# Kernel tuning notes

Measured on AMD Instinct MI355X. Metric: run time of the kernel, lower is better.

Reference implementation:

```python
import jax, jax.numpy as jnp
import numpy as np

N_NODES = 50000
N_RAND_EDGES = 800000  # plus N_NODES self-loop edges appended in setup
IN_FEATS, N_HIDDEN, N_CLASSES = 128, 64, 64


def setup_inputs() -> dict:
    key = jax.random.key(0)
    kf, ks, kd, k1, k2, k3 = jax.random.split(key, 6)
    features = jax.random.normal(kf, (N_NODES, IN_FEATS), dtype=jnp.float32)
    src = jax.random.randint(ks, (N_RAND_EDGES,), 0, N_NODES, dtype=jnp.int32)
    dst = jax.random.randint(kd, (N_RAND_EDGES,), 0, N_NODES, dtype=jnp.int32)
    # dgl.add_self_loop: append (i, i) for every node
    loop = jnp.arange(N_NODES, dtype=jnp.int32)
    src = jnp.concatenate([src, loop])
    dst = jnp.concatenate([dst, loop])

    def glorot(k, fan_in, fan_out):
        lim = jnp.sqrt(6.0 / (fan_in + fan_out)).astype(jnp.float32)
        return jax.random.uniform(k, (fan_in, fan_out), jnp.float32, -lim, lim)

    return {
        "features": features, "src": src, "dst": dst,
        "W1": glorot(k1, IN_FEATS, N_HIDDEN), "b1": jnp.zeros((N_HIDDEN,), jnp.float32),
        "W2": glorot(k2, N_HIDDEN, N_HIDDEN), "b2": jnp.zeros((N_HIDDEN,), jnp.float32),
        "W3": glorot(k3, N_HIDDEN, N_CLASSES), "b3": jnp.zeros((N_CLASSES,), jnp.float32),
    }


def _graph_conv(x, W, b, src, dst, norm_src_e, norm_dst_n, n_nodes):
    """DGL GraphConv, norm='both': D_dst^{-1/2} A D_src^{-1/2} X W + b, then relu."""
    if W.shape[0] > W.shape[1]:  # mult by W first when it shrinks the feature dim
        x = x @ W
        m = x[src] * norm_src_e[:, None]                      # [E, out]
        h = jax.ops.segment_sum(m, dst, num_segments=n_nodes)  # [N, out]
        h = h * norm_dst_n[:, None]
    else:
        m = x[src] * norm_src_e[:, None]                      # [E, in]
        h = jax.ops.segment_sum(m, dst, num_segments=n_nodes)  # [N, in]
        h = (h * norm_dst_n[:, None]) @ W
    return jax.nn.relu(h + b)


def reference(features, src, dst, W1, b1, W2, b2, W3, b3):
    n = features.shape[0]
    ones = jnp.ones(src.shape[0], dtype=features.dtype)
    out_deg = jax.ops.segment_sum(ones, src, num_segments=n)
    in_deg = jax.ops.segment_sum(ones, dst, num_segments=n)
    norm_out = jnp.where(out_deg > 0, jax.lax.rsqrt(jnp.maximum(out_deg, 1.0)), 0.0)
    norm_in = jnp.where(in_deg > 0, jax.lax.rsqrt(jnp.maximum(in_deg, 1.0)), 0.0)
    norm_src_e = norm_out[src]  # per-edge source normalization

    h1 = _graph_conv(features, W1, b1, src, dst, norm_src_e, norm_in, n)
    h2 = _graph_conv(h1, W2, b2, src, dst, norm_src_e, norm_in, n)
    h3 = _graph_conv(h2, W3, b3, src, dst, norm_src_e, norm_in, n)
    # JumpingKnowledge mode='max': elementwise max over stacked layer outputs
    return jnp.max(jnp.stack([h1, h2, h3], axis=0), axis=0)
```

## Files before the change

### kernel.cpp

```cpp
#include <hip/hip_runtime.h>

typedef _Float16 h16;
typedef __attribute__((ext_vector_type(4))) _Float16 half4;
typedef __attribute__((ext_vector_type(8))) _Float16 half8;
typedef __attribute__((ext_vector_type(8))) float float8;

#define RANGES 8
#define PPR    32
#define HTHREADS 1024
#define BINS   6400
#define HALF   (BINS / 2)
#define HWORDS (BINS)

__global__ __launch_bounds__(HTHREADS) void hist_kernel(const int* __restrict__ src,
                                                        const int* __restrict__ dst,
                                                        int* __restrict__ partial, int E) {
  __shared__ int h[HWORDS];
  const int r = blockIdx.x >> 5;
  const int c = blockIdx.x & 31;
  for (int i = threadIdx.x; i < HWORDS; i += HTHREADS) h[i] = 0;
  __syncthreads();
  const int lo = r * BINS;
  const int chunk = (E + PPR - 1) / PPR;
  const int e0 = c * chunk;
  const int e1 = min(E, e0 + chunk);
  for (int e = e0 + threadIdx.x; e < e1; e += HTHREADS) {
    int s = src[e] - lo;
    if ((unsigned)s < (unsigned)BINS) atomicAdd(&h[s >> 1], 1 << ((s & 1) * 16));
    int d = dst[e] - lo;
    if ((unsigned)d < (unsigned)BINS) atomicAdd(&h[HALF + (d >> 1)], 1 << ((d & 1) * 16));
  }
  __syncthreads();
  int* op = partial + (size_t)blockIdx.x * HWORDS;
  for (int i = threadIdx.x; i < HWORDS; i += HTHREADS) op[i] = h[i];
}

__global__ __launch_bounds__(256) void reduce_norm_scan1(
    int* __restrict__ partial, float* __restrict__ nout, float* __restrict__ nin,
    int* __restrict__ rowptr, int* __restrict__ bsums, int N) {
  __shared__ int s[256];
  const int j = blockIdx.x * 256 + threadIdx.x;
  const int r = j / HALF;
  const int w = j % HALF;
  int* base = partial + (size_t)(r * PPR) * HWORDS;
  int sumO = 0, runI = 0;
#pragma unroll 8
  for (int p = 0; p < PPR; ++p) {
    sumO += base[(size_t)p * HWORDS + w];
    int vI = base[(size_t)p * HWORDS + HALF + w];
    base[(size_t)p * HWORDS + HALF + w] = runI;
    runI += vI;
  }
  const int od0 = sumO & 0xFFFF, od1 = (sumO >> 16) & 0xFFFF;
  const int id0 = runI & 0xFFFF, id1 = (runI >> 16) & 0xFFFF;
  const int n0 = 2 * j, n1 = 2 * j + 1;
  if (n0 < N) {
    nout[n0] = od0 > 0 ? rsqrtf((float)od0) : 0.f;
    nin[n0]  = id0 > 0 ? rsqrtf((float)id0) : 0.f;
  }
  if (n1 < N) {
    nout[n1] = od1 > 0 ? rsqrtf((float)od1) : 0.f;
    nin[n1]  = id1 > 0 ? rsqrtf((float)id1) : 0.f;
  }
  const int local = id0 + id1;
  int v = local;
  s[threadIdx.x] = v;
  __syncthreads();
#pragma unroll
  for (int off = 1; off < 256; off <<= 1) {
    int tv = 0;
    if (threadIdx.x >= off) tv = s[threadIdx.x - off];
    __syncthreads();
    if (threadIdx.x >= off) s[threadIdx.x] += tv;
    __syncthreads();
  }
  const int excl = s[threadIdx.x] - v;
  if (n0 < N) rowptr[n0] = excl;
  if (n1 < N) rowptr[n1] = excl + id0;
  if (threadIdx.x == 255) bsums[blockIdx.x] = s[255];
}

__global__ __launch_bounds__(512) void add_off2(int* __restrict__ rowptr,
                                                const int* __restrict__ bsums,
                                                int N, int E, int nb) {
  __shared__ int s[128];
  const int tid = threadIdx.x;
  if (tid < 128) s[tid] = (tid < nb) ? bsums[tid] : 0;
  __syncthreads();
#pragma unroll
  for (int off = 1; off < 128; off <<= 1) {
    int v = 0;
    if (tid < 128 && tid >= off) v = s[tid - off];
    __syncthreads();
    if (tid < 128 && tid >= off) s[tid] += v;
    __syncthreads();
  }
  const int base = (blockIdx.x == 0) ? 0 : s[blockIdx.x - 1];
  const int i = blockIdx.x * 512 + tid;
  if (i < N) rowptr[i] += base;
  if (blockIdx.x == 0 && tid == 0) rowptr[N] = E;
}

__global__ __launch_bounds__(HTHREADS) void fill_kernel(
    const int* __restrict__ src, const int* __restrict__ dst,
    const int* __restrict__ rowptr, const int* __restrict__ partial,
    int* __restrict__ csr, int N, int E) {
  __shared__ int cur[BINS];
  const int r = blockIdx.x & 7;
  const int c = blockIdx.x >> 3;
  const int lo = r * BINS;
  const int* pf = partial + (size_t)(r * PPR + c) * HWORDS + HALF;
  for (int n = threadIdx.x; n < BINS; n += HTHREADS) {
    int g = lo + n;
    int rp = (g < N) ? rowptr[g] : 0;
    int pw = pf[n >> 1];
    cur[n] = rp + ((pw >> ((n & 1) * 16)) & 0xFFFF);
  }
  __syncthreads();
  const int chunk = (E + PPR - 1) / PPR;
  const int e0 = c * chunk;
  const int e1 = min(E, e0 + chunk);
  for (int e = e0 + threadIdx.x; e < e1; e += HTHREADS) {
    int d = dst[e] - lo;
    if ((unsigned)d < (unsigned)BINS) {
      int pos = atomicAdd(&cur[d], 1);
      csr[pos] = src[e];
    }
  }
}

__device__ __forceinline__ float8 gather_row(const int* __restrict__ rowptr,
                                             const int* __restrict__ csr,
                                             const half8* __restrict__ xv,
                                             int node, int lane) {
  const int b = rowptr[node], e = rowptr[node + 1];
  float8 a0 = 0.f, a1 = 0.f, a2 = 0.f, a3 = 0.f;
  int i = b;
  for (; i + 4 <= e; i += 4) {
    int s0 = csr[i + 0], s1 = csr[i + 1], s2 = csr[i + 2], s3 = csr[i + 3];
    half8 v0 = xv[(size_t)s0 * 8 + lane];
    half8 v1 = xv[(size_t)s1 * 8 + lane];
    half8 v2 = xv[(size_t)s2 * 8 + lane];
    half8 v3 = xv[(size_t)s3 * 8 + lane];
#pragma unroll
    for (int j = 0; j < 8; ++j) {
      a0[j] += (float)v0[j]; a1[j] += (float)v1[j];
      a2[j] += (float)v2[j]; a3[j] += (float)v3[j];
    }
  }
  for (; i < e; ++i) {
    int s = csr[i];
    half8 v = xv[(size_t)s * 8 + lane];
#pragma unroll
    for (int j = 0; j < 8; ++j) a0[j] += (float)v[j];
  }
#pragma unroll
  for (int j = 0; j < 8; ++j) a0[j] = (a0[j] + a1[j]) + (a2[j] + a3[j]);
  return a0;
}

__global__ __launch_bounds__(512) void agg1_kernel(
    const int* __restrict__ rowptr, const int* __restrict__ csr,
    const h16* __restrict__ x, const float* __restrict__ nin,
    const float* __restrict__ bias, const float* __restrict__ nout,
    half8* __restrict__ y, float* __restrict__ out, int N) {
  int t = blockIdx.x * 512 + threadIdx.x;
  int node = t >> 3;
  if (node >= N) return;
  int lane = t & 7;
  float8 acc = gather_row(rowptr, csr, reinterpret_cast<const half8*>(x), node, lane);
  const float s = nin[node];
  const float no = nout[node];
  float8 h;
  half8 hv;
#pragma unroll
  for (int j = 0; j < 8; ++j) {
    h[j] = fmaxf(acc[j] * s + bias[lane * 8 + j], 0.f);
    hv[j] = (h16)(h[j] * no);
  }
  float4 o0 = make_float4(h[0], h[1], h[2], h[3]);
  float4 o1 = make_float4(h[4], h[5], h[6], h[7]);
  size_t off = (size_t)node * 64 + lane * 8;
  *reinterpret_cast<float4*>(out + off)     = o0;
  *reinterpret_cast<float4*>(out + off + 4) = o1;
  y[(size_t)node * 8 + lane] = hv;
}

template <bool WRITEC>
__global__ __launch_bounds__(512) void fused_layer(
    const int* __restrict__ rowptr, const int* __restrict__ csr,
    const h16* __restrict__ x, const float* __restrict__ W,
    const float* __restrict__ nin, const float* __restrict__ bias,
    const float* __restrict__ nout,
    half4* __restrict__ C, float* __restrict__ out, int N) {
  __shared__ float sA[64][68];
  __shared__ float sB[64][64];
  const int t = threadIdx.x;
  const int row0 = blockIdx.x * 64;

  for (int i = t * 4; i < 64 * 64; i += 512 * 4)
    *reinterpret_cast<float4*>(&sB[0][0] + i) = *reinterpret_cast<const float4*>(W + i);

  {
    const int node = t >> 3, lane = t & 7;
    const int g = row0 + node;
    float8 acc = 0.f;
    float s = 0.f;
    if (g < N) {
      acc = gather_row(rowptr, csr, reinterpret_cast<const half8*>(x), g, lane);
      s = nin[g];
    }
    float4 w0 = make_float4(acc[0] * s, acc[1] * s, acc[2] * s, acc[3] * s);
    float4 w1 = make_float4(acc[4] * s, acc[5] * s, acc[6] * s, acc[7] * s);
    *reinterpret_cast<float4*>(&sA[node][lane * 8])     = w0;
    *reinterpret_cast<float4*>(&sA[node][lane * 8 + 4]) = w1;
  }
  __syncthreads();

  const int tx = t & 15;
  const int ry = t >> 4;
  const int r0 = 2 * ry, r1 = 2 * ry + 1;
  float4 acc0 = make_float4(0.f, 0.f, 0.f, 0.f);
  float4 acc1 = make_float4(0.f, 0.f, 0.f, 0.f);
#pragma unroll 8
  for (int k = 0; k < 64; ++k) {
    float a0 = sA[r0][k], a1 = sA[r1][k];
    float4 b = *reinterpret_cast<float4*>(&sB[k][tx * 4]);
    acc0.x += a0 * b.x; acc0.y += a0 * b.y; acc0.z += a0 * b.z; acc0.w += a0 * b.w;
    acc1.x += a1 * b.x; acc1.y += a1 * b.y; acc1.z += a1 * b.z; acc1.w += a1 * b.w;
  }

  const float4 bb = *reinterpret_cast<const float4*>(bias + tx * 4);
#pragma unroll
  for (int rr = 0; rr < 2; ++rr) {
    const int gr = row0 + (rr ? r1 : r0);
    if (gr >= N) continue;
    float4 v = rr ? acc1 : acc0;
    v.x = fmaxf(v.x + bb.x, 0.f);
    v.y = fmaxf(v.y + bb.y, 0.f);
    v.z = fmaxf(v.z + bb.z, 0.f);
    v.w = fmaxf(v.w + bb.w, 0.f);
    size_t off = (size_t)gr * 64 + tx * 4;
    float4 o = *reinterpret_cast<float4*>(out + off);
    o.x = fmaxf(o.x, v.x);
    o.y = fmaxf(o.y, v.y);
    o.z = fmaxf(o.z, v.z);
    o.w = fmaxf(o.w, v.w);
    *reinterpret_cast<float4*>(out + off) = o;
    if (WRITEC) {
      float no = nout[gr];
      half4 hv;
      hv.x = (h16)(v.x * no); hv.y = (h16)(v.y * no);
      hv.z = (h16)(v.z * no); hv.w = (h16)(v.w * no);
      C[(size_t)gr * 16 + tx] = hv;
    }
  }
}

__global__ __launch_bounds__(256) void gemm1_kernel(
    const float* __restrict__ A, const float* __restrict__ B,
    const float* __restrict__ nout, half4* __restrict__ C, int M) {
  __shared__ float sA[64][132];
  __shared__ float sB[128][64];
  const int t = threadIdx.x;
  const int row0 = blockIdx.x * 64;

  for (int i = t * 4; i < 64 * 128; i += 256 * 4) {
    int r = i / 128, c = i % 128;
    int gr = row0 + r;
    float4 v = make_float4(0.f, 0.f, 0.f, 0.f);
    if (gr < M) v = *reinterpret_cast<const float4*>(A + (size_t)gr * 128 + c);
    *reinterpret_cast<float4*>(&sA[r][c]) = v;
  }
  for (int i = t * 4; i < 128 * 64; i += 256 * 4)
    *reinterpret_cast<float4*>(&sB[0][0] + i) = *reinterpret_cast<const float4*>(B + i);
  __syncthreads();

  const int ty = t >> 4;
  const int tx = t & 15;
  float acc[4][4] = {};
#pragma unroll 8
  for (int k = 0; k < 128; ++k) {
    float a[4];
#pragma unroll
    for (int i = 0; i < 4; ++i) a[i] = sA[ty * 4 + i][k];
    float4 b = *reinterpret_cast<float4*>(&sB[k][tx * 4]);
#pragma unroll
    for (int i = 0; i < 4; ++i) {
      acc[i][0] += a[i] * b.x;
      acc[i][1] += a[i] * b.y;
      acc[i][2] += a[i] * b.z;
      acc[i][3] += a[i] * b.w;
    }
  }

#pragma unroll
  for (int i = 0; i < 4; ++i) {
    int gr = row0 + ty * 4 + i;
    if (gr >= M) continue;
    float no = nout[gr];
    half4 hv;
    hv.x = (h16)(acc[i][0] * no); hv.y = (h16)(acc[i][1] * no);
    hv.z = (h16)(acc[i][2] * no); hv.w = (h16)(acc[i][3] * no);
    C[(size_t)gr * 16 + tx] = hv;
  }
}

extern "C" void kernel_launch(void* const* d_in, const int* in_sizes, int n_in,
                              void* d_out, int out_size, void* d_ws, size_t ws_size,
                              hipStream_t stream) {
  const float* feat = (const float*)d_in[0];
  const int* src    = (const int*)d_in[1];
  const int* dst    = (const int*)d_in[2];
  const float* W1   = (const float*)d_in[3];
  const float* b1   = (const float*)d_in[4];
  const float* W2   = (const float*)d_in[5];
  const float* b2   = (const float*)d_in[6];
  const float* W3   = (const float*)d_in[7];
  const float* b3   = (const float*)d_in[8];
  float* out = (float*)d_out;

  const int N = in_sizes[0] / 128;
  const int E = in_sizes[1];

  char* p = (char*)d_ws;
  float* nout   = (float*)p;          p += (size_t)N * 4;
  float* nin    = (float*)p;          p += (size_t)N * 4;
  int*   rowptr = (int*)p;            p += ((size_t)N + 8) * 4;
  int*   bsums  = (int*)p;            p += 1024 * 4;
  int*   csr    = (int*)p;            p += (size_t)E * 4;
  p = (char*)(((uintptr_t)p + 15) & ~(uintptr_t)15);
  h16*   bufAh  = (h16*)p;            p += (size_t)N * 64 * 2;
  h16*   bufBh  = (h16*)p;            p += (size_t)N * 64 * 2;
  int*   partial = (int*)bufAh;

  const int nwords = RANGES * HALF;
  const int nb = nwords / 256;

  hist_kernel<<<RANGES * PPR, HTHREADS, 0, stream>>>(src, dst, partial, E);
  reduce_norm_scan1<<<nb, 256, 0, stream>>>(partial, nout, nin, rowptr, bsums, N);
  add_off2<<<nb, 512, 0, stream>>>(rowptr, bsums, N, E, nb);
  fill_kernel<<<RANGES * PPR, HTHREADS, 0, stream>>>(src, dst, rowptr, partial, csr, N, E);

  const int gemm_blocks  = (N + 63) / 64;
  const int agg1_blocks  = (int)(((size_t)N * 8 + 511) / 512);

  gemm1_kernel<<<gemm_blocks, 256, 0, stream>>>(feat, W1, nout, (half4*)bufAh, N);
  agg1_kernel<<<agg1_blocks, 512, 0, stream>>>(rowptr, csr, bufAh, nin, b1, nout,
                                               (half8*)bufBh, out, N);

  fused_layer<true><<<gemm_blocks, 512, 0, stream>>>(rowptr, csr, bufBh, W2, nin, b2, nout,
                                                     (half4*)bufAh, out, N);

  fused_layer<false><<<gemm_blocks, 512, 0, stream>>>(rowptr, csr, bufAh, W3, nin, b3, nullptr,
                                                      nullptr, out, N);
}
```

Before: 167.3 us.

## Merge all stages into one cooperative persistent kernel with grid syncs

Replaces the eight separate kernel launches (histogram, reduce/scan, offset add, CSR fill, GEMM1, aggregation and two fused layers) with a single cooperative kernel of 256 blocks × 1024 threads that runs each stage as a phase separated by grid.sync(). Stages now loop over tiles persistently, and the layer phases use 128-row tiles. The goal is to remove launch gaps and per-kernel ramp-up. In exchange, the fixed small grid may under-occupy the GPU, 1024-thread blocks limit register use, and each grid-wide barrier has its own cost.

```diff
diff --git a/kernel.cpp b/kernel.cpp
--- a/kernel.cpp
+++ b/kernel.cpp
@@ -1,4 +1,7 @@
 #include <hip/hip_runtime.h>
+#include <hip/hip_cooperative_groups.h>
+
+namespace cg = cooperative_groups;
 
 typedef _Float16 h16;
 typedef __attribute__((ext_vector_type(4))) _Float16 half4;
@@ -7,127 +10,22 @@
 
 #define RANGES 8
 #define PPR    32
-#define HTHREADS 1024
 #define BINS   6400
 #define HALF   (BINS / 2)
 #define HWORDS (BINS)
-
-__global__ __launch_bounds__(HTHREADS) void hist_kernel(const int* __restrict__ src,
-                                                        const int* __restrict__ dst,
-                                                        int* __restrict__ partial, int E) {
-  __shared__ int h[HWORDS];
-  const int r = blockIdx.x >> 5;
-  const int c = blockIdx.x & 31;
-  for (int i = threadIdx.x; i < HWORDS; i += HTHREADS) h[i] = 0;
-  __syncthreads();
-  const int lo = r * BINS;
-  const int chunk = (E + PPR - 1) / PPR;
-  const int e0 = c * chunk;
-  const int e1 = min(E, e0 + chunk);
-  for (int e = e0 + threadIdx.x; e < e1; e += HTHREADS) {
-    int s = src[e] - lo;
-    if ((unsigned)s < (unsigned)BINS) atomicAdd(&h[s >> 1], 1 << ((s & 1) * 16));
-    int d = dst[e] - lo;
-    if ((unsigned)d < (unsigned)BINS) atomicAdd(&h[HALF + (d >> 1)], 1 << ((d & 1) * 16));
-  }
-  __syncthreads();
-  int* op = partial + (size_t)blockIdx.x * HWORDS;
-  for (int i = threadIdx.x; i < HWORDS; i += HTHREADS) op[i] = h[i];
-}
-
-__global__ __launch_bounds__(256) void reduce_norm_scan1(
-    int* __restrict__ partial, float* __restrict__ nout, float* __restrict__ nin,
-    int* __restrict__ rowptr, int* __restrict__ bsums, int N) {
-  __shared__ int s[256];
-  const int j = blockIdx.x * 256 + threadIdx.x;
-  const int r = j / HALF;
-  const int w = j % HALF;
-  int* base = partial + (size_t)(r * PPR) * HWORDS;
-  int sumO = 0, runI = 0;
-#pragma unroll 8
-  for (int p = 0; p < PPR; ++p) {
-    sumO += base[(size_t)p * HWORDS + w];
-    int vI = base[(size_t)p * HWORDS + HALF + w];
-    base[(size_t)p * HWORDS + HALF + w] = runI;
-    runI += vI;
-  }
-  const int od0 = sumO & 0xFFFF, od1 = (sumO >> 16) & 0xFFFF;
-  const int id0 = runI & 0xFFFF, id1 = (runI >> 16) & 0xFFFF;
-  const int n0 = 2 * j, n1 = 2 * j + 1;
-  if (n0 < N) {
-    nout[n0] = od0 > 0 ? rsqrtf((float)od0) : 0.f;
-    nin[n0]  = id0 > 0 ? rsqrtf((float)id0) : 0.f;
-  }
-  if (n1 < N) {
-    nout[n1] = od1 > 0 ? rsqrtf((float)od1) : 0.f;
-    nin[n1]  = id1 > 0 ? rsqrtf((float)id1) : 0.f;
-  }
-  const int local = id0 + id1;
-  int v = local;
-  s[threadIdx.x] = v;
-  __syncthreads();
-#pragma unroll
-  for (int off = 1; off < 256; off <<= 1) {
-    int tv = 0;
-    if (threadIdx.x >= off) tv = s[threadIdx.x - off];
-    __syncthreads();
-    if (threadIdx.x >= off) s[threadIdx.x] += tv;
-    __syncthreads();
-  }
-  const int excl = s[threadIdx.x] - v;
-  if (n0 < N) rowptr[n0] = excl;
-  if (n1 < N) rowptr[n1] = excl + id0;
-  if (threadIdx.x == 255) bsums[blockIdx.x] = s[255];
-}
-
-__global__ __launch_bounds__(512) void add_off2(int* __restrict__ rowptr,
-                                                const int* __restrict__ bsums,
-                                                int N, int E, int nb) {
-  __shared__ int s[128];
-  const int tid = threadIdx.x;
-  if (tid < 128) s[tid] = (tid < nb) ? bsums[tid] : 0;
-  __syncthreads();
-#pragma unroll
-  for (int off = 1; off < 128; off <<= 1) {
-    int v = 0;
-    if (tid < 128 && tid >= off) v = s[tid - off];
-    __syncthreads();
-    if (tid < 128 && tid >= off) s[tid] += v;
-    __syncthreads();
-  }
-  const int base = (blockIdx.x == 0) ? 0 : s[blockIdx.x - 1];
-  const int i = blockIdx.x * 512 + tid;
-  if (i < N) rowptr[i] += base;
-  if (blockIdx.x == 0 && tid == 0) rowptr[N] = E;
-}
-
-__global__ __launch_bounds__(HTHREADS) void fill_kernel(
-    const int* __restrict__ src, const int* __restrict__ dst,
-    const int* __restrict__ rowptr, const int* __restrict__ partial,
-    int* __restrict__ csr, int N, int E) {
-  __shared__ int cur[BINS];
-  const int r = blockIdx.x & 7;
-  const int c = blockIdx.x >> 3;
-  const int lo = r * BINS;
-  const int* pf = partial + (size_t)(r * PPR + c) * HWORDS + HALF;
-  for (int n = threadIdx.x; n < BINS; n += HTHREADS) {
-    int g = lo + n;
-    int rp = (g < N) ? rowptr[g] : 0;
-    int pw = pf[n >> 1];
-    cur[n] = rp + ((pw >> ((n & 1) * 16)) & 0xFFFF);
-  }
-  __syncthreads();
-  const int chunk = (E + PPR - 1) / PPR;
-  const int e0 = c * chunk;
-  const int e1 = min(E, e0 + chunk);
-  for (int e = e0 + threadIdx.x; e < e1; e += HTHREADS) {
-    int d = dst[e] - lo;
-    if ((unsigned)d < (unsigned)BINS) {
-      int pos = atomicAdd(&cur[d], 1);
-      csr[pos] = src[e];
-    }
-  }
-}
+#define NTHREADS 1024
+#define NBLOCKS  256
+#define SMEM_BYTES (128 * 68 * 4 + 64 * 64 * 4)
+
+struct Params {
+  const float* feat; const int* src; const int* dst;
+  const float* W1; const float* b1; const float* W2; const float* b2;
+  const float* W3; const float* b3;
+  float* out;
+  float* nout; float* nin; int* rowptr; int* bsums; int* csr;
+  h16* bufAh; h16* bufBh; int* partial;
+  int N; int E;
+};
 
 __device__ __forceinline__ float8 gather_row(const int* __restrict__ rowptr,
                                              const int* __restrict__ csr,
@@ -159,199 +57,294 @@
   return a0;
 }
 
-__global__ __launch_bounds__(512) void agg1_kernel(
-    const int* __restrict__ rowptr, const int* __restrict__ csr,
-    const h16* __restrict__ x, const float* __restrict__ nin,
-    const float* __restrict__ bias, const float* __restrict__ nout,
-    half8* __restrict__ y, float* __restrict__ out, int N) {
-  int t = blockIdx.x * 512 + threadIdx.x;
-  int node = t >> 3;
-  if (node >= N) return;
-  int lane = t & 7;
-  float8 acc = gather_row(rowptr, csr, reinterpret_cast<const half8*>(x), node, lane);
-  const float s = nin[node];
-  const float no = nout[node];
-  float8 h;
-  half8 hv;
-#pragma unroll
-  for (int j = 0; j < 8; ++j) {
-    h[j] = fmaxf(acc[j] * s + bias[lane * 8 + j], 0.f);
-    hv[j] = (h16)(h[j] * no);
-  }
-  float4 o0 = make_float4(h[0], h[1], h[2], h[3]);
-  float4 o1 = make_float4(h[4], h[5], h[6], h[7]);
-  size_t off = (size_t)node * 64 + lane * 8;
-  *reinterpret_cast<float4*>(out + off)     = o0;
-  *reinterpret_cast<float4*>(out + off + 4) = o1;
-  y[(size_t)node * 8 + lane] = hv;
-}
-
 template <bool WRITEC>
-__global__ __launch_bounds__(512) void fused_layer(
-    const int* __restrict__ rowptr, const int* __restrict__ csr,
-    const h16* __restrict__ x, const float* __restrict__ W,
-    const float* __restrict__ nin, const float* __restrict__ bias,
-    const float* __restrict__ nout,
-    half4* __restrict__ C, float* __restrict__ out, int N) {
-  __shared__ float sA[64][68];
-  __shared__ float sB[64][64];
-  const int t = threadIdx.x;
-  const int row0 = blockIdx.x * 64;
-
-  for (int i = t * 4; i < 64 * 64; i += 512 * 4)
-    *reinterpret_cast<float4*>(&sB[0][0] + i) = *reinterpret_cast<const float4*>(W + i);
-
-  {
-    const int node = t >> 3, lane = t & 7;
+__device__ void fused_phase(const Params& P, char* smem_raw,
+                            const h16* __restrict__ x, const float* __restrict__ W,
+                            const float* __restrict__ bias, half4* __restrict__ C) {
+  float* fA = (float*)smem_raw;
+  float* fB = fA + 128 * 68;
+  const int N = P.N;
+  const int tid = threadIdx.x;
+  const int ntiles = (N + 127) >> 7;
+  {
+    int i = tid * 4;
+    *reinterpret_cast<float4*>(fB + i) = *reinterpret_cast<const float4*>(W + i);
+  }
+  for (int tile = blockIdx.x; tile < ntiles; tile += NBLOCKS) {
+    __syncthreads();
+    const int row0 = tile << 7;
+    const int node = tid >> 3, lane = tid & 7;
     const int g = row0 + node;
     float8 acc = 0.f;
     float s = 0.f;
     if (g < N) {
-      acc = gather_row(rowptr, csr, reinterpret_cast<const half8*>(x), g, lane);
-      s = nin[g];
+      acc = gather_row(P.rowptr, P.csr, reinterpret_cast<const half8*>(x), g, lane);
+      s = P.nin[g];
     }
     float4 w0 = make_float4(acc[0] * s, acc[1] * s, acc[2] * s, acc[3] * s);
     float4 w1 = make_float4(acc[4] * s, acc[5] * s, acc[6] * s, acc[7] * s);
-    *reinterpret_cast<float4*>(&sA[node][lane * 8])     = w0;
-    *reinterpret_cast<float4*>(&sA[node][lane * 8 + 4]) = w1;
-  }
-  __syncthreads();
-
-  const int tx = t & 15;
-  const int ry = t >> 4;
-  const int r0 = 2 * ry, r1 = 2 * ry + 1;
-  float4 acc0 = make_float4(0.f, 0.f, 0.f, 0.f);
-  float4 acc1 = make_float4(0.f, 0.f, 0.f, 0.f);
+    *reinterpret_cast<float4*>(fA + node * 68 + lane * 8)     = w0;
+    *reinterpret_cast<float4*>(fA + node * 68 + lane * 8 + 4) = w1;
+    __syncthreads();
+
+    const int tx = tid & 15;
+    const int ry = tid >> 4;
+    const int r0 = 2 * ry, r1 = r0 + 1;
+    float4 a0 = make_float4(0.f, 0.f, 0.f, 0.f);
+    float4 a1 = make_float4(0.f, 0.f, 0.f, 0.f);
 #pragma unroll 8
-  for (int k = 0; k < 64; ++k) {
-    float a0 = sA[r0][k], a1 = sA[r1][k];
-    float4 b = *reinterpret_cast<float4*>(&sB[k][tx * 4]);
-    acc0.x += a0 * b.x; acc0.y += a0 * b.y; acc0.z += a0 * b.z; acc0.w += a0 * b.w;
-    acc1.x += a1 * b.x; acc1.y += a1 * b.y; acc1.z += a1 * b.z; acc1.w += a1 * b.w;
-  }
-
-  const float4 bb = *reinterpret_cast<const float4*>(bias + tx * 4);
-#pragma unroll
-  for (int rr = 0; rr < 2; ++rr) {
-    const int gr = row0 + (rr ? r1 : r0);
-    if (gr >= N) continue;
-    float4 v = rr ? acc1 : acc0;
-    v.x = fmaxf(v.x + bb.x, 0.f);
-    v.y = fmaxf(v.y + bb.y, 0.f);
-    v.z = fmaxf(v.z + bb.z, 0.f);
-    v.w = fmaxf(v.w + bb.w, 0.f);
-    size_t off = (size_t)gr * 64 + tx * 4;
-    float4 o = *reinterpret_cast<float4*>(out + off);
-    o.x = fmaxf(o.x, v.x);
-    o.y = fmaxf(o.y, v.y);
-    o.z = fmaxf(o.z, v.z);
-    o.w = fmaxf(o.w, v.w);
-    *reinterpret_cast<float4*>(out + off) = o;
-    if (WRITEC) {
-      float no = nout[gr];
-      half4 hv;
-      hv.x = (h16)(v.x * no); hv.y = (h16)(v.y * no);
-      hv.z = (h16)(v.z * no); hv.w = (h16)(v.w * no);
-      C[(size_t)gr * 16 + tx] = hv;
+    for (int k = 0; k < 64; ++k) {
+      float x0 = fA[r0 * 68 + k], x1 = fA[r1 * 68 + k];
+      float4 b = *reinterpret_cast<float4*>(fB + k * 64 + tx * 4);
+      a0.x += x0 * b.x; a0.y += x0 * b.y; a0.z += x0 * b.z; a0.w += x0 * b.w;
+      a1.x += x1 * b.x; a1.y += x1 * b.y; a1.z += x1 * b.z; a1.w += x1 * b.w;
+    }
+    const float4 bb = *reinterpret_cast<const float4*>(bias + tx * 4);
+#pragma unroll
+    for (int rr = 0; rr < 2; ++rr) {
+      const int gr = row0 + (rr ? r1 : r0);
+      if (gr >= N) continue;
+      float4 v = rr ? a1 : a0;
+      v.x = fmaxf(v.x + bb.x, 0.f);
+      v.y = fmaxf(v.y + bb.y, 0.f);
+      v.z = fmaxf(v.z + bb.z, 0.f);
+      v.w = fmaxf(v.w + bb.w, 0.f);
+      size_t off = (size_t)gr * 64 + tx * 4;
+      float4 o = *reinterpret_cast<float4*>(P.out + off);
+      o.x = fmaxf(o.x, v.x);
+      o.y = fmaxf(o.y, v.y);
+      o.z = fmaxf(o.z, v.z);
+      o.w = fmaxf(o.w, v.w);
+      *reinterpret_cast<float4*>(P.out + off) = o;
+      if (WRITEC) {
+        float no = P.nout[gr];
+        half4 hv;
+        hv.x = (h16)(v.x * no); hv.y = (h16)(v.y * no);
+        hv.z = (h16)(v.z * no); hv.w = (h16)(v.w * no);
+        C[(size_t)gr * 16 + tx] = hv;
+      }
     }
   }
 }
 
-__global__ __launch_bounds__(256) void gemm1_kernel(
-    const float* __restrict__ A, const float* __restrict__ B,
-    const float* __restrict__ nout, half4* __restrict__ C, int M) {
-  __shared__ float sA[64][132];
-  __shared__ float sB[128][64];
-  const int t = threadIdx.x;
-  const int row0 = blockIdx.x * 64;
-
-  for (int i = t * 4; i < 64 * 128; i += 256 * 4) {
-    int r = i / 128, c = i % 128;
-    int gr = row0 + r;
-    float4 v = make_float4(0.f, 0.f, 0.f, 0.f);
-    if (gr < M) v = *reinterpret_cast<const float4*>(A + (size_t)gr * 128 + c);
-    *reinterpret_cast<float4*>(&sA[r][c]) = v;
-  }
-  for (int i = t * 4; i < 128 * 64; i += 256 * 4)
-    *reinterpret_cast<float4*>(&sB[0][0] + i) = *reinterpret_cast<const float4*>(B + i);
-  __syncthreads();
-
-  const int ty = t >> 4;
-  const int tx = t & 15;
-  float acc[4][4] = {};
+__global__ __launch_bounds__(NTHREADS) void mega(Params P) {
+  extern __shared__ char smem_raw[];
+  cg::grid_group grid = cg::this_grid();
+  const int bid = blockIdx.x, tid = threadIdx.x;
+  const int N = P.N, E = P.E;
+  const int chunk = (E + PPR - 1) / PPR;
+
+  {
+    int* h = (int*)smem_raw;
+    const int r = bid >> 5, c = bid & 31;
+    for (int i = tid; i < HWORDS; i += NTHREADS) h[i] = 0;
+    __syncthreads();
+    const int lo = r * BINS;
+    const int e0 = c * chunk, e1 = min(E, e0 + chunk);
+    for (int e = e0 + tid; e < e1; e += NTHREADS) {
+      int s = P.src[e] - lo;
+      if ((unsigned)s < (unsigned)BINS) atomicAdd(&h[s >> 1], 1 << ((s & 1) * 16));
+      int d = P.dst[e] - lo;
+      if ((unsigned)d < (unsigned)BINS) atomicAdd(&h[HALF + (d >> 1)], 1 << ((d & 1) * 16));
+    }
+    __syncthreads();
+    int* op = P.partial + (size_t)bid * HWORDS;
+    for (int i = tid; i < HWORDS; i += NTHREADS) op[i] = h[i];
+  }
+  grid.sync();
+
+  {
+    int* s = (int*)smem_raw;
+    const bool active = (bid < 100) && (tid < 256);
+    int id0 = 0, id1 = 0;
+    if (active) {
+      const int j = bid * 256 + tid;
+      const int r = j / HALF, w = j % HALF;
+      int* base = P.partial + (size_t)(r * PPR) * HWORDS;
+      int sumO = 0, runI = 0;
 #pragma unroll 8
-  for (int k = 0; k < 128; ++k) {
-    float a[4];
-#pragma unroll
-    for (int i = 0; i < 4; ++i) a[i] = sA[ty * 4 + i][k];
-    float4 b = *reinterpret_cast<float4*>(&sB[k][tx * 4]);
-#pragma unroll
-    for (int i = 0; i < 4; ++i) {
-      acc[i][0] += a[i] * b.x;
-      acc[i][1] += a[i] * b.y;
-      acc[i][2] += a[i] * b.z;
-      acc[i][3] += a[i] * b.w;
-    }
-  }
-
-#pragma unroll
-  for (int i = 0; i < 4; ++i) {
-    int gr = row0 + ty * 4 + i;
-    if (gr >= M) continue;
-    float no = nout[gr];
-    half4 hv;
-    hv.x = (h16)(acc[i][0] * no); hv.y = (h16)(acc[i][1] * no);
-    hv.z = (h16)(acc[i][2] * no); hv.w = (h16)(acc[i][3] * no);
-    C[(size_t)gr * 16 + tx] = hv;
-  }
+      for (int p = 0; p < PPR; ++p) {
+        sumO += base[(size_t)p * HWORDS + w];
+        int vI = base[(size_t)p * HWORDS + HALF + w];
+        base[(size_t)p * HWORDS + HALF + w] = runI;
+        runI += vI;
+      }
+      const int od0 = sumO & 0xFFFF, od1 = (sumO >> 16) & 0xFFFF;
+      id0 = runI & 0xFFFF; id1 = (runI >> 16) & 0xFFFF;
+      const int n0 = 2 * j, n1 = n0 + 1;
+      if (n0 < N) {
+        P.nout[n0] = od0 > 0 ? rsqrtf((float)od0) : 0.f;
+        P.nin[n0]  = id0 > 0 ? rsqrtf((float)id0) : 0.f;
+      }
+      if (n1 < N) {
+        P.nout[n1] = od1 > 0 ? rsqrtf((float)od1) : 0.f;
+        P.nin[n1]  = id1 > 0 ? rsqrtf((float)id1) : 0.f;
+      }
+    }
+    if (tid < 256) s[tid] = active ? (id0 + id1) : 0;
+    __syncthreads();
+#pragma unroll
+    for (int off = 1; off < 256; off <<= 1) {
+      int tv = 0;
+      if (tid < 256 && tid >= off) tv = s[tid - off];
+      __syncthreads();
+      if (tid < 256 && tid >= off) s[tid] += tv;
+      __syncthreads();
+    }
+    if (active) {
+      const int j = bid * 256 + tid;
+      const int excl = s[tid] - (id0 + id1);
+      const int n0 = 2 * j, n1 = n0 + 1;
+      if (n0 < N) P.rowptr[n0] = excl;
+      if (n1 < N) P.rowptr[n1] = excl + id0;
+    }
+    if (bid < 100 && tid == 255) P.bsums[bid] = s[255];
+  }
+  grid.sync();
+
+  {
+    int* top = (int*)smem_raw;
+    if (tid < 128) top[tid] = (tid < 100) ? P.bsums[tid] : 0;
+    __syncthreads();
+#pragma unroll
+    for (int off = 1; off < 128; off <<= 1) {
+      int v = 0;
+      if (tid < 128 && tid >= off) v = top[tid - off];
+      __syncthreads();
+      if (tid < 128 && tid >= off) top[tid] += v;
+      __syncthreads();
+    }
+    const int i = bid * NTHREADS + tid;
+    if (i < N) {
+      const int v = i >> 9;
+      const int base = v ? top[v - 1] : 0;
+      P.rowptr[i] += base;
+    }
+    if (bid == 0 && tid == 0) P.rowptr[N] = E;
+  }
+  grid.sync();
+
+  {
+    int* cur = (int*)smem_raw;
+    const int r = bid & 7, c = bid >> 3;
+    const int lo = r * BINS;
+    const int* pf = P.partial + (size_t)(r * PPR + c) * HWORDS + HALF;
+    for (int n = tid; n < BINS; n += NTHREADS) {
+      int g = lo + n;
+      int rp = (g < N) ? P.rowptr[g] : 0;
+      int pw = pf[n >> 1];
+      cur[n] = rp + ((pw >> ((n & 1) * 16)) & 0xFFFF);
+    }
+    __syncthreads();
+    const int e0 = c * chunk, e1 = min(E, e0 + chunk);
+    for (int e = e0 + tid; e < e1; e += NTHREADS) {
+      int d = P.dst[e] - lo;
+      if ((unsigned)d < (unsigned)BINS) {
+        int pos = atomicAdd(&cur[d], 1);
+        P.csr[pos] = P.src[e];
+      }
+    }
+  }
+  grid.sync();
+
+  {
+    float* sA = (float*)smem_raw;
+    float* sB = sA + 64 * 68;
+    const int ntiles = (N + 63) >> 6;
+    const int ry = tid >> 4;
+    const int tx = tid & 15;
+    for (int tile = bid; tile < ntiles; tile += NBLOCKS) {
+      const int row0 = tile << 6;
+      float4 acc = make_float4(0.f, 0.f, 0.f, 0.f);
+#pragma unroll
+      for (int kc = 0; kc < 2; ++kc) {
+        __syncthreads();
+        {
+          const int i = tid * 4, r = i >> 6, c = i & 63;
+          const int gr = row0 + r;
+          float4 v = make_float4(0.f, 0.f, 0.f, 0.f);
+          if (gr < N) v = *reinterpret_cast<const float4*>(P.feat + (size_t)gr * 128 + kc * 64 + c);
+          *reinterpret_cast<float4*>(sA + r * 68 + c) = v;
+        }
+        {
+          const int i = tid * 4, r = i >> 6, c = i & 63;
+          *reinterpret_cast<float4*>(sB + r * 64 + c) =
+              *reinterpret_cast<const float4*>(P.W1 + (size_t)(kc * 64 + r) * 64 + c);
+        }
+        __syncthreads();
+#pragma unroll 8
+        for (int k = 0; k < 64; ++k) {
+          float a = sA[ry * 68 + k];
+          float4 b = *reinterpret_cast<float4*>(sB + k * 64 + tx * 4);
+          acc.x += a * b.x; acc.y += a * b.y; acc.z += a * b.z; acc.w += a * b.w;
+        }
+      }
+      const int gr = row0 + ry;
+      if (gr < N) {
+        float no = P.nout[gr];
+        half4 hv;
+        hv.x = (h16)(acc.x * no); hv.y = (h16)(acc.y * no);
+        hv.z = (h16)(acc.z * no); hv.w = (h16)(acc.w * no);
+        reinterpret_cast<half4*>(P.bufAh)[(size_t)gr * 16 + tx] = hv;
+      }
+    }
+  }
+  grid.sync();
+
+  {
+    const int total = N * 8;
+    for (int t = bid * NTHREADS + tid; t < total; t += NBLOCKS * NTHREADS) {
+      const int node = t >> 3, lane = t & 7;
+      float8 acc = gather_row(P.rowptr, P.csr, reinterpret_cast<const half8*>(P.bufAh), node, lane);
+      const float s = P.nin[node];
+      const float no = P.nout[node];
+      float8 h;
+      half8 hv;
+#pragma unroll
+      for (int j = 0; j < 8; ++j) {
+        h[j] = fmaxf(acc[j] * s + P.b1[lane * 8 + j], 0.f);
+        hv[j] = (h16)(h[j] * no);
+      }
+      size_t off = (size_t)node * 64 + lane * 8;
+      *reinterpret_cast<float4*>(P.out + off)     = make_float4(h[0], h[1], h[2], h[3]);
+      *reinterpret_cast<float4*>(P.out + off + 4) = make_float4(h[4], h[5], h[6], h[7]);
+      reinterpret_cast<half8*>(P.bufBh)[(size_t)node * 8 + lane] = hv;
+    }
+  }
+  grid.sync();
+
+  fused_phase<true>(P, smem_raw, P.bufBh, P.W2, P.b2, reinterpret_cast<half4*>(P.bufAh));
+  grid.sync();
+
+  fused_phase<false>(P, smem_raw, P.bufAh, P.W3, P.b3, nullptr);
 }
 
 extern "C" void kernel_launch(void* const* d_in, const int* in_sizes, int n_in,
                               void* d_out, int out_size, void* d_ws, size_t ws_size,
                               hipStream_t stream) {
-  const float* feat = (const float*)d_in[0];
-  const int* src    = (const int*)d_in[1];
-  const int* dst    = (const int*)d_in[2];
-  const float* W1   = (const float*)d_in[3];
-  const float* b1   = (const float*)d_in[4];
-  const float* W2   = (const float*)d_in[5];
-  const float* b2   = (const float*)d_in[6];
-  const float* W3   = (const float*)d_in[7];
-  const float* b3   = (const float*)d_in[8];
-  float* out = (float*)d_out;
-
-  const int N = in_sizes[0] / 128;
-  const int E = in_sizes[1];
+  Params P;
+  P.feat = (const float*)d_in[0];
+  P.src  = (const int*)d_in[1];
+  P.dst  = (const int*)d_in[2];
+  P.W1 = (const float*)d_in[3]; P.b1 = (const float*)d_in[4];
+  P.W2 = (const float*)d_in[5]; P.b2 = (const float*)d_in[6];
+  P.W3 = (const float*)d_in[7]; P.b3 = (const float*)d_in[8];
+  P.out = (float*)d_out;
+  P.N = in_sizes[0] / 128;
+  P.E = in_sizes[1];
 
   char* p = (char*)d_ws;
-  float* nout   = (float*)p;          p += (size_t)N * 4;
-  float* nin    = (float*)p;          p += (size_t)N * 4;
-  int*   rowptr = (int*)p;            p += ((size_t)N + 8) * 4;
-  int*   bsums  = (int*)p;            p += 1024 * 4;
-  int*   csr    = (int*)p;            p += (size_t)E * 4;
+  P.nout   = (float*)p;   p += (size_t)P.N * 4;
+  P.nin    = (float*)p;   p += (size_t)P.N * 4;
+  P.rowptr = (int*)p;     p += ((size_t)P.N + 8) * 4;
+  P.bsums  = (int*)p;     p += 1024 * 4;
+  P.csr    = (int*)p;     p += (size_t)P.E * 4;
   p = (char*)(((uintptr_t)p + 15) & ~(uintptr_t)15);
-  h16*   bufAh  = (h16*)p;            p += (size_t)N * 64 * 2;
-  h16*   bufBh  = (h16*)p;            p += (size_t)N * 64 * 2;
-  int*   partial = (int*)bufAh;
-
-  const int nwords = RANGES * HALF;
-  const int nb = nwords / 256;
-
-  hist_kernel<<<RANGES * PPR, HTHREADS, 0, stream>>>(src, dst, partial, E);
-  reduce_norm_scan1<<<nb, 256, 0, stream>>>(partial, nout, nin, rowptr, bsums, N);
-  add_off2<<<nb, 512, 0, stream>>>(rowptr, bsums, N, E, nb);
-  fill_kernel<<<RANGES * PPR, HTHREADS, 0, stream>>>(src, dst, rowptr, partial, csr, N, E);
-
-  const int gemm_blocks  = (N + 63) / 64;
-  const int agg1_blocks  = (int)(((size_t)N * 8 + 511) / 512);
-
-  gemm1_kernel<<<gemm_blocks, 256, 0, stream>>>(feat, W1, nout, (half4*)bufAh, N);
-  agg1_kernel<<<agg1_blocks, 512, 0, stream>>>(rowptr, csr, bufAh, nin, b1, nout,
-                                               (half8*)bufBh, out, N);
-
-  fused_layer<true><<<gemm_blocks, 512, 0, stream>>>(rowptr, csr, bufBh, W2, nin, b2, nout,
-                                                     (half4*)bufAh, out, N);
-
-  fused_layer<false><<<gemm_blocks, 512, 0, stream>>>(rowptr, csr, bufAh, W3, nin, b3, nullptr,
-                                                      nullptr, out, N);
+  P.bufAh  = (h16*)p;     p += (size_t)P.N * 64 * 2;
+  P.bufBh  = (h16*)p;     p += (size_t)P.N * 64 * 2;
+  P.partial = (int*)P.bufAh;
+
+  void* args[] = { &P };
+  hipLaunchCooperativeKernel((const void*)mega, dim3(NBLOCKS), dim3(NTHREADS),
+                             args, SMEM_BYTES, stream);
 }
```

Result: slower. 398.1 us (+137.9%).

## Fold scan offset into fill kernel, use 16-bit CSR indices, double histogram partitions

Applied to the files above, without the earlier changes.

Removes the separate add_off2 launch: fill_kernel now scans the block sums itself and writes absolute row pointers into a new buffer. CSR source indices are stored as unsigned short, which halves index traffic during the three gathers; this relies on N fitting in 16 bits (50000 does). Histogram partitions per range go from 32 to 64, so there are more blocks with smaller edge chunks. The partial buffer moves to its own workspace region because it no longer fits inside bufAh.

```diff
diff --git a/kernel.cpp b/kernel.cpp
--- a/kernel.cpp
+++ b/kernel.cpp
@@ -6,18 +6,19 @@
 typedef __attribute__((ext_vector_type(8))) float float8;
 
 #define RANGES 8
-#define PPR    32
+#define PPR    64
 #define HTHREADS 1024
 #define BINS   6400
 #define HALF   (BINS / 2)
 #define HWORDS (BINS)
+#define NSEG   100
 
 __global__ __launch_bounds__(HTHREADS) void hist_kernel(const int* __restrict__ src,
                                                         const int* __restrict__ dst,
                                                         int* __restrict__ partial, int E) {
   __shared__ int h[HWORDS];
-  const int r = blockIdx.x >> 5;
-  const int c = blockIdx.x & 31;
+  const int r = blockIdx.x >> 6;
+  const int c = blockIdx.x & 63;
   for (int i = threadIdx.x; i < HWORDS; i += HTHREADS) h[i] = 0;
   __syncthreads();
   const int lo = r * BINS;
@@ -53,7 +54,7 @@
   }
   const int od0 = sumO & 0xFFFF, od1 = (sumO >> 16) & 0xFFFF;
   const int id0 = runI & 0xFFFF, id1 = (runI >> 16) & 0xFFFF;
-  const int n0 = 2 * j, n1 = 2 * j + 1;
+  const int n0 = 2 * j, n1 = n0 + 1;
   if (n0 < N) {
     nout[n0] = od0 > 0 ? rsqrtf((float)od0) : 0.f;
     nin[n0]  = id0 > 0 ? rsqrtf((float)id0) : 0.f;
@@ -80,57 +81,55 @@
   if (threadIdx.x == 255) bsums[blockIdx.x] = s[255];
 }
 
-__global__ __launch_bounds__(512) void add_off2(int* __restrict__ rowptr,
-                                                const int* __restrict__ bsums,
-                                                int N, int E, int nb) {
-  __shared__ int s[128];
+__global__ __launch_bounds__(HTHREADS) void fill_kernel(
+    const int* __restrict__ src, const int* __restrict__ dst,
+    const int* __restrict__ rowptr, const int* __restrict__ bsums,
+    const int* __restrict__ partial, int* __restrict__ rowptr_abs,
+    unsigned short* __restrict__ csr, int N, int E) {
+  __shared__ int cur[BINS];
+  __shared__ int top[128];
   const int tid = threadIdx.x;
-  if (tid < 128) s[tid] = (tid < nb) ? bsums[tid] : 0;
+  const int r = blockIdx.x & 7;
+  const int c = blockIdx.x >> 3;
+  if (tid < 128) top[tid] = (tid < NSEG) ? bsums[tid] : 0;
   __syncthreads();
 #pragma unroll
   for (int off = 1; off < 128; off <<= 1) {
     int v = 0;
-    if (tid < 128 && tid >= off) v = s[tid - off];
+    if (tid < 128 && tid >= off) v = top[tid - off];
     __syncthreads();
-    if (tid < 128 && tid >= off) s[tid] += v;
+    if (tid < 128 && tid >= off) top[tid] += v;
     __syncthreads();
   }
-  const int base = (blockIdx.x == 0) ? 0 : s[blockIdx.x - 1];
-  const int i = blockIdx.x * 512 + tid;
-  if (i < N) rowptr[i] += base;
-  if (blockIdx.x == 0 && tid == 0) rowptr[N] = E;
-}
-
-__global__ __launch_bounds__(HTHREADS) void fill_kernel(
-    const int* __restrict__ src, const int* __restrict__ dst,
-    const int* __restrict__ rowptr, const int* __restrict__ partial,
-    int* __restrict__ csr, int N, int E) {
-  __shared__ int cur[BINS];
-  const int r = blockIdx.x & 7;
-  const int c = blockIdx.x >> 3;
   const int lo = r * BINS;
   const int* pf = partial + (size_t)(r * PPR + c) * HWORDS + HALF;
-  for (int n = threadIdx.x; n < BINS; n += HTHREADS) {
+  for (int n = tid; n < BINS; n += HTHREADS) {
     int g = lo + n;
-    int rp = (g < N) ? rowptr[g] : 0;
+    int rp = 0;
+    if (g < N) {
+      int seg = g >> 9;
+      rp = rowptr[g] + (seg ? top[seg - 1] : 0);
+      if (c == 0) rowptr_abs[g] = rp;
+    }
     int pw = pf[n >> 1];
     cur[n] = rp + ((pw >> ((n & 1) * 16)) & 0xFFFF);
   }
+  if (blockIdx.x == 0 && tid == 0) rowptr_abs[N] = E;
   __syncthreads();
   const int chunk = (E + PPR - 1) / PPR;
   const int e0 = c * chunk;
   const int e1 = min(E, e0 + chunk);
-  for (int e = e0 + threadIdx.x; e < e1; e += HTHREADS) {
+  for (int e = e0 + tid; e < e1; e += HTHREADS) {
     int d = dst[e] - lo;
     if ((unsigned)d < (unsigned)BINS) {
       int pos = atomicAdd(&cur[d], 1);
-      csr[pos] = src[e];
+      csr[pos] = (unsigned short)src[e];
     }
   }
 }
 
 __device__ __forceinline__ float8 gather_row(const int* __restrict__ rowptr,
-                                             const int* __restrict__ csr,
+                                             const unsigned short* __restrict__ csr,
                                              const half8* __restrict__ xv,
                                              int node, int lane) {
   const int b = rowptr[node], e = rowptr[node + 1];
@@ -160,7 +159,7 @@
 }
 
 __global__ __launch_bounds__(512) void agg1_kernel(
-    const int* __restrict__ rowptr, const int* __restrict__ csr,
+    const int* __restrict__ rowptr, const unsigned short* __restrict__ csr,
     const h16* __restrict__ x, const float* __restrict__ nin,
     const float* __restrict__ bias, const float* __restrict__ nout,
     half8* __restrict__ y, float* __restrict__ out, int N) {
@@ -178,17 +177,15 @@
     h[j] = fmaxf(acc[j] * s + bias[lane * 8 + j], 0.f);
     hv[j] = (h16)(h[j] * no);
   }
-  float4 o0 = make_float4(h[0], h[1], h[2], h[3]);
-  float4 o1 = make_float4(h[4], h[5], h[6], h[7]);
   size_t off = (size_t)node * 64 + lane * 8;
-  *reinterpret_cast<float4*>(out + off)     = o0;
-  *reinterpret_cast<float4*>(out + off + 4) = o1;
+  *reinterpret_cast<float4*>(out + off)     = make_float4(h[0], h[1], h[2], h[3]);
+  *reinterpret_cast<float4*>(out + off + 4) = make_float4(h[4], h[5], h[6], h[7]);
   y[(size_t)node * 8 + lane] = hv;
 }
 
 template <bool WRITEC>
 __global__ __launch_bounds__(512) void fused_layer(
-    const int* __restrict__ rowptr, const int* __restrict__ csr,
+    const int* __restrict__ rowptr, const unsigned short* __restrict__ csr,
     const h16* __restrict__ x, const float* __restrict__ W,
     const float* __restrict__ nin, const float* __restrict__ bias,
     const float* __restrict__ nout,
@@ -210,24 +207,24 @@
       acc = gather_row(rowptr, csr, reinterpret_cast<const half8*>(x), g, lane);
       s = nin[g];
     }
-    float4 w0 = make_float4(acc[0] * s, acc[1] * s, acc[2] * s, acc[3] * s);
-    float4 w1 = make_float4(acc[4] * s, acc[5] * s, acc[6] * s, acc[7] * s);
-    *reinterpret_cast<float4*>(&sA[node][lane * 8])     = w0;
-    *reinterpret_cast<float4*>(&sA[node][lane * 8 + 4]) = w1;
+    *reinterpret_cast<float4*>(&sA[node][lane * 8]) =
+        make_float4(acc[0] * s, acc[1] * s, acc[2] * s, acc[3] * s);
+    *reinterpret_cast<float4*>(&sA[node][lane * 8 + 4]) =
+        make_float4(acc[4] * s, acc[5] * s, acc[6] * s, acc[7] * s);
   }
   __syncthreads();
 
   const int tx = t & 15;
   const int ry = t >> 4;
-  const int r0 = 2 * ry, r1 = 2 * ry + 1;
-  float4 acc0 = make_float4(0.f, 0.f, 0.f, 0.f);
-  float4 acc1 = make_float4(0.f, 0.f, 0.f, 0.f);
+  const int r0 = 2 * ry, r1 = r0 + 1;
+  float4 a0 = make_float4(0.f, 0.f, 0.f, 0.f);
+  float4 a1 = make_float4(0.f, 0.f, 0.f, 0.f);
 #pragma unroll 8
   for (int k = 0; k < 64; ++k) {
-    float a0 = sA[r0][k], a1 = sA[r1][k];
+    float x0 = sA[r0][k], x1 = sA[r1][k];
     float4 b = *reinterpret_cast<float4*>(&sB[k][tx * 4]);
-    acc0.x += a0 * b.x; acc0.y += a0 * b.y; acc0.z += a0 * b.z; acc0.w += a0 * b.w;
-    acc1.x += a1 * b.x; acc1.y += a1 * b.y; acc1.z += a1 * b.z; acc1.w += a1 * b.w;
+    a0.x += x0 * b.x; a0.y += x0 * b.y; a0.z += x0 * b.z; a0.w += x0 * b.w;
+    a1.x += x1 * b.x; a1.y += x1 * b.y; a1.z += x1 * b.z; a1.w += x1 * b.w;
   }
 
   const float4 bb = *reinterpret_cast<const float4*>(bias + tx * 4);
@@ -235,7 +232,7 @@
   for (int rr = 0; rr < 2; ++rr) {
     const int gr = row0 + (rr ? r1 : r0);
     if (gr >= N) continue;
-    float4 v = rr ? acc1 : acc0;
+    float4 v = rr ? a1 : a0;
     v.x = fmaxf(v.x + bb.x, 0.f);
     v.y = fmaxf(v.y + bb.y, 0.f);
     v.z = fmaxf(v.z + bb.z, 0.f);
@@ -324,34 +321,31 @@
   const int E = in_sizes[1];
 
   char* p = (char*)d_ws;
-  float* nout   = (float*)p;          p += (size_t)N * 4;
-  float* nin    = (float*)p;          p += (size_t)N * 4;
-  int*   rowptr = (int*)p;            p += ((size_t)N + 8) * 4;
-  int*   bsums  = (int*)p;            p += 1024 * 4;
-  int*   csr    = (int*)p;            p += (size_t)E * 4;
+  float* nout       = (float*)p;     p += (size_t)N * 4;
+  float* nin        = (float*)p;     p += (size_t)N * 4;
+  int*   rowptr     = (int*)p;       p += ((size_t)N + 8) * 4;
+  int*   rowptr_abs = (int*)p;       p += ((size_t)N + 8) * 4;
+  int*   bsums      = (int*)p;       p += 1024 * 4;
+  unsigned short* csr = (unsigned short*)p;  p += (((size_t)E + 8) & ~7) * 2;
   p = (char*)(((uintptr_t)p + 15) & ~(uintptr_t)15);
-  h16*   bufAh  = (h16*)p;            p += (size_t)N * 64 * 2;
-  h16*   bufBh  = (h16*)p;            p += (size_t)N * 64 * 2;
-  int*   partial = (int*)bufAh;
-
-  const int nwords = RANGES * HALF;
-  const int nb = nwords / 256;
+  h16*   bufAh = (h16*)p;            p += (size_t)N * 64 * 2;
+  h16*   bufBh = (h16*)p;            p += (size_t)N * 64 * 2;
+  p = (char*)(((uintptr_t)p + 15) & ~(uintptr_t)15);
+  int*   partial = (int*)p;          p += (size_t)RANGES * PPR * HWORDS * 4;
 
   hist_kernel<<<RANGES * PPR, HTHREADS, 0, stream>>>(src, dst, partial, E);
-  reduce_norm_scan1<<<nb, 256, 0, stream>>>(partial, nout, nin, rowptr, bsums, N);
-  add_off2<<<nb, 512, 0, stream>>>(rowptr, bsums, N, E, nb);
-  fill_kernel<<<RANGES * PPR, HTHREADS, 0, stream>>>(src, dst, rowptr, partial, csr, N, E);
-
-  const int gemm_blocks  = (N + 63) / 64;
-  const int agg1_blocks  = (int)(((size_t)N * 8 + 511) / 512);
+  reduce_norm_scan1<<<NSEG, 256, 0, stream>>>(partial, nout, nin, rowptr, bsums, N);
+  fill_kernel<<<RANGES * PPR, HTHREADS, 0, stream>>>(src, dst, rowptr, bsums, partial,
+                                                     rowptr_abs, csr, N, E);
+
+  const int gemm_blocks = (N + 63) / 64;
+  const int agg1_blocks = (int)(((size_t)N * 8 + 511) / 512);
 
   gemm1_kernel<<<gemm_blocks, 256, 0, stream>>>(feat, W1, nout, (half4*)bufAh, N);
-  agg1_kernel<<<agg1_blocks, 512, 0, stream>>>(rowptr, csr, bufAh, nin, b1, nout,
+  agg1_kernel<<<agg1_blocks, 512, 0, stream>>>(rowptr_abs, csr, bufAh, nin, b1, nout,
                                                (half8*)bufBh, out, N);
-
-  fused_layer<true><<<gemm_blocks, 512, 0, stream>>>(rowptr, csr, bufBh, W2, nin, b2, nout,
+  fused_layer<true><<<gemm_blocks, 512, 0, stream>>>(rowptr_abs, csr, bufBh, W2, nin, b2, nout,
                                                      (half4*)bufAh, out, N);
-
-  fused_layer<false><<<gemm_blocks, 512, 0, stream>>>(rowptr, csr, bufAh, W3, nin, b3, nullptr,
+  fused_layer<false><<<gemm_blocks, 512, 0, stream>>>(rowptr_abs, csr, bufAh, W3, nin, b3, nullptr,
                                                       nullptr, out, N);
 }
```

Result: faster. 154.4 us (-7.7%).
